# Kernel optimization log

Measured on AMD Instinct MI355X. Metric: run time of the kernel, lower is better.

Reference implementation:

```python
import jax, jax.numpy as jnp
import numpy as np
import math

NUM_HEADS = 8
FDIM = 64
NUM_BUCKETS = 32
MAX_DISTANCE = 128


def _relative_position_bucket(rel_pos, num_buckets=NUM_BUCKETS, max_distance=MAX_DISTANCE):
    nb = num_buckets // 2
    ret = (rel_pos >= 0).astype(jnp.int32) * nb
    n = jnp.abs(rel_pos)
    max_exact = nb // 2
    is_small = n < max_exact
    # safe log: clamp n to >=1 where large-branch is unused
    val_large = max_exact + (
        jnp.log(jnp.maximum(n, 1).astype(jnp.float32) / max_exact)
        / math.log(max_distance / max_exact) * (nb - max_exact)
    ).astype(jnp.int32)
    val_large = jnp.minimum(val_large, nb - 1)
    return ret + jnp.where(is_small, n, val_large)


def setup_inputs() -> dict:
    key = jax.random.key(0)
    k = jax.random.split(key, 5)
    B, Nin, F, T = 4, 64, FDIM, 1024
    N = NUM_HEADS * FDIM
    x = jax.random.normal(k[0], (B, Nin, F, T), dtype=jnp.float32)
    # kaiming_normal: std = 1/sqrt(fan_in)
    w_in = jax.random.normal(k[1], (NUM_HEADS, Nin), dtype=jnp.float32) / np.sqrt(Nin)
    w_qk = jax.random.normal(k[2], (2 * N, N), dtype=jnp.float32) / np.sqrt(N)
    w_out = jax.random.normal(k[3], (Nin, NUM_HEADS), dtype=jnp.float32) / np.sqrt(NUM_HEADS)
    rel_bias = jax.random.normal(k[4], (NUM_BUCKETS, NUM_HEADS), dtype=jnp.float32) * 0.02
    return {"x": x, "w_in": w_in, "w_qk": w_qk, "w_out": w_out, "rel_bias": rel_bias}


def reference(x, w_in, w_qk, w_out, rel_bias):
    B, Nin, F, T = x.shape
    h, f = NUM_HEADS, FDIM
    scale = f ** (-0.5)
    # proj_in: 1x1 conv2d Nin -> h
    xi = jnp.einsum('bcft,hc->bhft', x, w_in)          # [B,h,F,T]
    xr = xi.reshape(B, h * f, T)                        # b (h f) t
    v = xr.reshape(B, h, f, T).transpose(0, 1, 3, 2)    # [B,h,T,f]
    # qk: 1x1 conv1d N -> 2N
    qk = jnp.einsum('bct,dc->bdt', xr, w_qk)            # [B,2N,T]
    qk = qk.reshape(B, h, 2 * f, T).transpose(0, 1, 3, 2)  # [B,h,T,2f]
    q, k = qk[..., :f], qk[..., f:]
    sim = jnp.einsum('bhnd,bhmd->bhnm', q, k)           # [B,h,T,T]
    # relative position bias
    q_pos = jnp.arange(T)
    k_pos = jnp.arange(T)
    rel = k_pos[None, :] - q_pos[:, None]               # [T,T]
    buckets = _relative_position_bucket(rel)
    bias = rel_bias[buckets]                            # [T,T,h]
    bias = bias.transpose(2, 0, 1)[None]                # [1,h,T,T]
    sim = (sim + bias) * scale
    attn = jax.nn.softmax(sim, axis=-1)
    out = jnp.einsum('bhnm,bhmd->bhnd', attn, v)        # [B,h,T,f]
    out = out.transpose(0, 1, 3, 2)                     # [B,h,f,T]
    out = jnp.einsum('bhft,ch->bcft', out, w_out)       # [B,Nin,F,T]
    return out
```

## Files before the change

### kernel.cpp

```cpp
#include <hip/hip_runtime.h>
#include <math.h>

#define QSCALE 0.18033688011112042f

typedef __attribute__((ext_vector_type(4))) float  f32x4;
typedef __attribute__((ext_vector_type(2))) float  f32x2;
typedef __attribute__((ext_vector_type(8))) short  bf16x8;
typedef __attribute__((ext_vector_type(4))) short  bf16x4;
typedef __attribute__((ext_vector_type(4))) int    i32x4;

static __device__ __forceinline__ short f2bf(float f) {
    union { float f; unsigned u; } v; v.f = f;
    unsigned r = v.u + 0x7fffu + ((v.u >> 16) & 1u);
    return (short)(r >> 16);
}
static __device__ __forceinline__ int pk2bf(float a, float b) {
    return ((int)f2bf(a) & 0xffff) | ((int)f2bf(b) << 16);
}

#define MFMA16(A,B,C) __builtin_amdgcn_mfma_f32_16x16x32_bf16(A, B, C, 0, 0, 0)

__global__ void k_prep(const float* __restrict__ wqk, short* __restrict__ wqk_b) {
    int i = blockIdx.x * 256 + threadIdx.x;
    int D = i >> 9;
    float s = (D & 64) ? 1.0f : QSCALE;
    wqk_b[i] = f2bf(wqk[i] * s);
}

__global__ __launch_bounds__(256) void k_proj_in(
    const float* __restrict__ x, const float* __restrict__ w_in,
    short* __restrict__ xi_v, short* __restrict__ xr_t)
{
    __shared__ float w_s[512];
    __shared__ __align__(16) short tr[64 * 72];
    int tid = threadIdx.x;
    int tx = tid & 31, fy = tid >> 5;
    int tb = blockIdx.x, fb = blockIdx.y, b = blockIdx.z;
    w_s[tid] = w_in[tid & 511];
    w_s[(tid + 256) & 511] = w_in[(tid + 256) & 511];
    __syncthreads();

    int f = fb * 8 + fy;
    int t = tb * 64 + tx * 2;
    float acc[8][2];
    #pragma unroll
    for (int h = 0; h < 8; h++) { acc[h][0] = 0.f; acc[h][1] = 0.f; }

    const float* xp = x + ((size_t)b * 64 * 64 + (size_t)f) * 1024 + t;
    f32x2 buf[8];
    #pragma unroll
    for (int i = 0; i < 8; i++) buf[i] = *(const f32x2*)&xp[(size_t)i * 65536];
    #pragma unroll
    for (int c8 = 0; c8 < 64; c8 += 8) {
        f32x2 cur[8];
        #pragma unroll
        for (int i = 0; i < 8; i++) cur[i] = buf[i];
        if (c8 + 8 < 64) {
            #pragma unroll
            for (int i = 0; i < 8; i++)
                buf[i] = *(const f32x2*)&xp[(size_t)(c8 + 8 + i) * 65536];
        }
        #pragma unroll
        for (int i = 0; i < 8; i++)
            #pragma unroll
            for (int h = 0; h < 8; h++) {
                float wv = w_s[h * 64 + c8 + i];
                acc[h][0] = fmaf(cur[i][0], wv, acc[h][0]);
                acc[h][1] = fmaf(cur[i][1], wv, acc[h][1]);
            }
    }
    #pragma unroll
    for (int h = 0; h < 8; h++)
        *(int*)&xi_v[(((size_t)b * 8 + h) * 64 + f) * 1024 + t] = pk2bf(acc[h][0], acc[h][1]);
    #pragma unroll
    for (int h = 0; h < 8; h++) {
        tr[(tx * 2 + 0) * 72 + h * 8 + fy] = f2bf(acc[h][0]);
        tr[(tx * 2 + 1) * 72 + h * 8 + fy] = f2bf(acc[h][1]);
    }
    __syncthreads();
    int h2 = tid & 7, trow = tid >> 3;
    #pragma unroll
    for (int i = 0; i < 2; i++) {
        int t2 = trow + i * 32;
        i32x4 v = *(const i32x4*)&tr[t2 * 72 + h2 * 8];
        *(i32x4*)&xr_t[((size_t)b * 1024 + tb * 64 + t2) * 512 + h2 * 64 + fb * 8] = v;
    }
}

__global__ __launch_bounds__(256, 4) void k_qk(
    const short* __restrict__ wqk_b, const short* __restrict__ xr_t,
    short* __restrict__ qk_t)
{
    __shared__ __align__(16) short As[64 * 72];
    __shared__ __align__(16) short Bs[64 * 72];
    int tid = threadIdx.x;
    int w = tid >> 6, lane = tid & 63;
    int quad = lane >> 4, l16 = lane & 15;
    int t0 = blockIdx.x * 64;
    int Dt = blockIdx.y;
    int b  = blockIdx.z;

    f32x4 acc[4];
    #pragma unroll
    for (int tt = 0; tt < 4; tt++) acc[tt] = (f32x4){0.f,0.f,0.f,0.f};

    const short* Ag = wqk_b + (size_t)Dt * 64 * 512;
    const short* Bg = xr_t + ((size_t)b * 1024 + t0) * 512;

    int s_row = tid >> 2, s_col = (tid & 3) * 16;

    for (int kk = 0; kk < 512; kk += 64) {
        __syncthreads();
        #pragma unroll
        for (int i = 0; i < 2; i++) {
            *(i32x4*)&As[s_row * 72 + s_col + i * 8] =
                *(const i32x4*)&Ag[(size_t)s_row * 512 + kk + s_col + i * 8];
            *(i32x4*)&Bs[s_row * 72 + s_col + i * 8] =
                *(const i32x4*)&Bg[(size_t)s_row * 512 + kk + s_col + i * 8];
        }
        __syncthreads();
        bf16x8 af[2];
        #pragma unroll
        for (int kc = 0; kc < 2; kc++)
            af[kc] = *(const bf16x8*)&As[(w * 16 + l16) * 72 + kc * 32 + quad * 8];
        #pragma unroll
        for (int tt = 0; tt < 4; tt++) {
            bf16x8 bf0 = *(const bf16x8*)&Bs[(tt * 16 + l16) * 72 + quad * 8];
            bf16x8 bf1 = *(const bf16x8*)&Bs[(tt * 16 + l16) * 72 + 32 + quad * 8];
            acc[tt] = MFMA16(af[0], bf0, acc[tt]);
            acc[tt] = MFMA16(af[1], bf1, acc[tt]);
        }
    }
    int h = Dt >> 1;
    int d2 = (Dt & 1) * 64 + w * 16 + quad * 4;
    #pragma unroll
    for (int tt = 0; tt < 4; tt++) {
        bf16x4 pk;
        pk.x = f2bf(acc[tt][0]); pk.y = f2bf(acc[tt][1]);
        pk.z = f2bf(acc[tt][2]); pk.w = f2bf(acc[tt][3]);
        int t = t0 + tt * 16 + l16;
        *(bf16x4*)&qk_t[(((size_t)b * 8 + h) * 1024 + t) * 128 + d2] = pk;
    }
}

__global__ __launch_bounds__(256, 4) void k_attn(
    const short* __restrict__ qk_t, const short* __restrict__ xi_v,
    const float* __restrict__ rel_bias, float* __restrict__ o_part,
    float* __restrict__ lsum)
{
    __shared__ __align__(16) short Ks[64 * 72];
    __shared__ __align__(16) short Vs[64 * 72];
    __shared__ __align__(16) short Ps[4][16 * 72];
    __shared__ float elut[2048];
    int tid = threadIdx.x;
    int w = tid >> 6, lane = tid & 63;
    int quad = lane >> 4, l16 = lane & 15;
    int nb = blockIdx.x, bh = blockIdx.y, mh = blockIdx.z;
    int h = bh & 7;
    int n_base = nb * 64;

    for (int i = tid; i < 2047; i += 256) {
        int rel = i - 1023;
        int ret = (rel >= 0) ? 16 : 0;
        int na = rel < 0 ? -rel : rel;
        int idx;
        if (na < 8) idx = ret + na;
        else {
            int vl = 8 + (int)(log2f((float)na * 0.125f) * 2.0f);
            vl = vl > 15 ? 15 : vl;
            idx = ret + vl;
        }
        elut[i] = exp2f(rel_bias[idx * 8 + h] * QSCALE);
    }

    const short* qb = qk_t + (size_t)bh * (1024 * 128);
    const short* vb = xi_v + (size_t)bh * (64 * 1024);

    bf16x8 qf[2];
    #pragma unroll
    for (int kk = 0; kk < 2; kk++)
        qf[kk] = *(const bf16x8*)&qb[(size_t)(n_base + w * 16 + l16) * 128 + kk * 32 + quad * 8];

    f32x4 acc_o[4];
    #pragma unroll
    for (int dt = 0; dt < 4; dt++) acc_o[dt] = (f32x4){0.f,0.f,0.f,0.f};
    float l_st = 0.f;

    int srow = tid >> 2;
    int soff = (tid & 3) * 16;
    int m0 = mh * 512;
    i32x4 gk[2], gv[2];
    #pragma unroll
    for (int i = 0; i < 2; i++) {
        gk[i] = *(const i32x4*)&qb[(size_t)(m0 + srow) * 128 + 64 + soff + i * 8];
        gv[i] = *(const i32x4*)&vb[(size_t)srow * 1024 + m0 + soff + i * 8];
    }

    __syncthreads();

    #pragma unroll 1
    for (int it = 0; it < 8; it++) {
        *(i32x4*)&Ks[srow * 72 + soff]     = gk[0];
        *(i32x4*)&Ks[srow * 72 + soff + 8] = gk[1];
        *(i32x4*)&Vs[srow * 72 + soff]     = gv[0];
        *(i32x4*)&Vs[srow * 72 + soff + 8] = gv[1];
        __syncthreads();
        if (it < 7) {
            int m1 = m0 + 64;
            #pragma unroll
            for (int i = 0; i < 2; i++) {
                gk[i] = *(const i32x4*)&qb[(size_t)(m1 + srow) * 128 + 64 + soff + i * 8];
                gv[i] = *(const i32x4*)&vb[(size_t)srow * 1024 + m1 + soff + i * 8];
            }
        }

        f32x4 s[4];
        #pragma unroll
        for (int mt = 0; mt < 4; mt++) {
            bf16x8 kf0 = *(const bf16x8*)&Ks[(mt * 16 + l16) * 72 + quad * 8];
            bf16x8 kf1 = *(const bf16x8*)&Ks[(mt * 16 + l16) * 72 + 32 + quad * 8];
            f32x4 tacc = (f32x4){0.f,0.f,0.f,0.f};
            tacc = MFMA16(kf0, qf[0], tacc);
            tacc = MFMA16(kf1, qf[1], tacc);
            s[mt] = tacc;
        }

        int n = n_base + w * 16 + l16;
        #pragma unroll
        for (int mt = 0; mt < 4; mt++) {
            int rel0 = m0 + mt * 16 + quad * 4 - n + 1023;
            #pragma unroll
            for (int j = 0; j < 4; j++) {
                float p = exp2f(s[mt][j]) * elut[rel0 + j];
                s[mt][j] = p;
                l_st += p;
            }
        }
        #pragma unroll
        for (int mt = 0; mt < 4; mt++) {
            bf16x4 pk;
            pk.x = f2bf(s[mt][0]); pk.y = f2bf(s[mt][1]);
            pk.z = f2bf(s[mt][2]); pk.w = f2bf(s[mt][3]);
            *(bf16x4*)&Ps[w][l16 * 72 + mt * 16 + quad * 4] = pk;
        }
        #pragma unroll
        for (int si = 0; si < 2; si++) {
            bf16x8 pf = *(const bf16x8*)&Ps[w][l16 * 72 + si * 32 + quad * 8];
            #pragma unroll
            for (int dt = 0; dt < 4; dt++) {
                bf16x8 vf = *(const bf16x8*)&Vs[(dt * 16 + l16) * 72 + si * 32 + quad * 8];
                acc_o[dt] = MFMA16(pf, vf, acc_o[dt]);
            }
        }
        m0 += 64;
        __syncthreads();
    }
    #pragma unroll
    for (int dt = 0; dt < 4; dt++)
        *(f32x4*)&o_part[(((size_t)mh * 32 + bh) * 64 + dt * 16 + l16) * 1024 + n_base + w * 16 + quad * 4] = acc_o[dt];
    l_st += __shfl_xor(l_st, 16);
    l_st += __shfl_xor(l_st, 32);
    if (quad == 0)
        lsum[((size_t)bh * 2 + mh) * 1024 + n_base + w * 16 + l16] = l_st;
}

__global__ __launch_bounds__(512) void k_proj_out(
    const float* __restrict__ o_part, const float* __restrict__ lsum,
    const float* __restrict__ w_out, float* __restrict__ out)
{
    __shared__ float w_s[512];
    __shared__ float o_s[8][64];
    int tid = threadIdx.x;
    int tx = tid & 63, ty = tid >> 6;
    int tb = blockIdx.x, f = blockIdx.y, b = blockIdx.z;
    w_s[tid] = w_out[tid];
    int t = tb * 64 + tx;
    int bh = b * 8 + ty;
    float l0 = lsum[((size_t)bh * 2 + 0) * 1024 + t];
    float l1 = lsum[((size_t)bh * 2 + 1) * 1024 + t];
    float o0 = o_part[((size_t)(0 * 32 + bh) * 64 + f) * 1024 + t];
    float o1 = o_part[((size_t)(1 * 32 + bh) * 64 + f) * 1024 + t];
    o_s[ty][tx] = (o0 + o1) / (l0 + l1);
    __syncthreads();
    float ov[8];
    #pragma unroll
    for (int hh = 0; hh < 8; hh++) ov[hh] = o_s[hh][tx];
    #pragma unroll
    for (int j = 0; j < 8; j++) {
        int c = ty * 8 + j;
        float a = 0.f;
        #pragma unroll
        for (int hh = 0; hh < 8; hh++) a = fmaf(ov[hh], w_s[c * 8 + hh], a);
        out[(((size_t)b * 64 + c) * 64 + f) * 1024 + t] = a;
    }
}

extern "C" void kernel_launch(void* const* d_in, const int* in_sizes, int n_in,
                              void* d_out, int out_size, void* d_ws, size_t ws_size,
                              hipStream_t stream)
{
    const float* x        = (const float*)d_in[0];
    const float* w_in     = (const float*)d_in[1];
    const float* w_qk     = (const float*)d_in[2];
    const float* w_out    = (const float*)d_in[3];
    const float* rel_bias = (const float*)d_in[4];
    float* out = (float*)d_out;

    char* ws = (char*)d_ws;
    short* wqk_b  = (short*)(ws);
    short* xi_v   = (short*)(ws + (size_t)1  * (1 << 20));
    short* xr_t   = (short*)(ws + (size_t)5  * (1 << 20));
    short* qk_t   = (short*)(ws + (size_t)9  * (1 << 20));
    float* o_part = (float*)(ws + (size_t)17 * (1 << 20));
    float* lsum   = (float*)(ws + (size_t)33 * (1 << 20));

    hipLaunchKernelGGL(k_prep,     dim3(2048),       dim3(256), 0, stream, w_qk, wqk_b);
    hipLaunchKernelGGL(k_proj_in,  dim3(16, 8, 4),   dim3(256), 0, stream, x, w_in, xi_v, xr_t);
    hipLaunchKernelGGL(k_qk,       dim3(16, 16, 4),  dim3(256), 0, stream, wqk_b, xr_t, qk_t);
    hipLaunchKernelGGL(k_attn,     dim3(16, 32, 2),  dim3(256), 0, stream, qk_t, xi_v, rel_bias, o_part, lsum);
    hipLaunchKernelGGL(k_proj_out, dim3(16, 64, 4),  dim3(512), 0, stream, o_part, lsum, w_out, out);
}
```

Baseline: 162.2 us.

## Fuse weight bf16 conversion into QK GEMM and drop attention key-split

Removes the separate weight-prep kernel by converting fp32 w_qk to scaled bf16 inside the QK GEMM's shared-memory load. The attention kernel no longer splits keys into two halves. Each block now loops over all 1024 keys and normalizes its output by the row sum itself. A remapped 1D grid with an XCD-aware block swizzle replaces the 3D grid. This cuts one launch, the partial-output write/read and the combine step in proj_out. In exchange the attention grid halves to 512 blocks and each block's serial loop gets longer.

```diff
diff --git a/kernel.cpp b/kernel.cpp
--- a/kernel.cpp
+++ b/kernel.cpp
@@ -19,13 +19,6 @@
 }
 
 #define MFMA16(A,B,C) __builtin_amdgcn_mfma_f32_16x16x32_bf16(A, B, C, 0, 0, 0)
-
-__global__ void k_prep(const float* __restrict__ wqk, short* __restrict__ wqk_b) {
-    int i = blockIdx.x * 256 + threadIdx.x;
-    int D = i >> 9;
-    float s = (D & 64) ? 1.0f : QSCALE;
-    wqk_b[i] = f2bf(wqk[i] * s);
-}
 
 __global__ __launch_bounds__(256) void k_proj_in(
     const float* __restrict__ x, const float* __restrict__ w_in,
@@ -88,7 +81,7 @@
 }
 
 __global__ __launch_bounds__(256, 4) void k_qk(
-    const short* __restrict__ wqk_b, const short* __restrict__ xr_t,
+    const float* __restrict__ wqk, const short* __restrict__ xr_t,
     short* __restrict__ qk_t)
 {
     __shared__ __align__(16) short As[64 * 72];
@@ -104,20 +97,28 @@
     #pragma unroll
     for (int tt = 0; tt < 4; tt++) acc[tt] = (f32x4){0.f,0.f,0.f,0.f};
 
-    const short* Ag = wqk_b + (size_t)Dt * 64 * 512;
+    int s_row = tid >> 2, s_col = (tid & 3) * 16;
+    const float* Ag = wqk + ((size_t)Dt * 64 + s_row) * 512;
     const short* Bg = xr_t + ((size_t)b * 1024 + t0) * 512;
-
-    int s_row = tid >> 2, s_col = (tid & 3) * 16;
+    float s = (Dt & 1) ? 1.0f : QSCALE;
 
     for (int kk = 0; kk < 512; kk += 64) {
         __syncthreads();
-        #pragma unroll
-        for (int i = 0; i < 2; i++) {
-            *(i32x4*)&As[s_row * 72 + s_col + i * 8] =
-                *(const i32x4*)&Ag[(size_t)s_row * 512 + kk + s_col + i * 8];
-            *(i32x4*)&Bs[s_row * 72 + s_col + i * 8] =
-                *(const i32x4*)&Bg[(size_t)s_row * 512 + kk + s_col + i * 8];
-        }
+        f32x4 a0 = *(const f32x4*)&Ag[kk + s_col];
+        f32x4 a1 = *(const f32x4*)&Ag[kk + s_col + 4];
+        f32x4 a2 = *(const f32x4*)&Ag[kk + s_col + 8];
+        f32x4 a3 = *(const f32x4*)&Ag[kk + s_col + 12];
+        i32x4 w0, w1;
+        w0[0] = pk2bf(a0[0]*s, a0[1]*s); w0[1] = pk2bf(a0[2]*s, a0[3]*s);
+        w0[2] = pk2bf(a1[0]*s, a1[1]*s); w0[3] = pk2bf(a1[2]*s, a1[3]*s);
+        w1[0] = pk2bf(a2[0]*s, a2[1]*s); w1[1] = pk2bf(a2[2]*s, a2[3]*s);
+        w1[2] = pk2bf(a3[0]*s, a3[1]*s); w1[3] = pk2bf(a3[2]*s, a3[3]*s);
+        *(i32x4*)&As[s_row * 72 + s_col]     = w0;
+        *(i32x4*)&As[s_row * 72 + s_col + 8] = w1;
+        *(i32x4*)&Bs[s_row * 72 + s_col] =
+            *(const i32x4*)&Bg[(size_t)s_row * 512 + kk + s_col];
+        *(i32x4*)&Bs[s_row * 72 + s_col + 8] =
+            *(const i32x4*)&Bg[(size_t)s_row * 512 + kk + s_col + 8];
         __syncthreads();
         bf16x8 af[2];
         #pragma unroll
@@ -145,8 +146,7 @@
 
 __global__ __launch_bounds__(256, 4) void k_attn(
     const short* __restrict__ qk_t, const short* __restrict__ xi_v,
-    const float* __restrict__ rel_bias, float* __restrict__ o_part,
-    float* __restrict__ lsum)
+    const float* __restrict__ rel_bias, float* __restrict__ o_n)
 {
     __shared__ __align__(16) short Ks[64 * 72];
     __shared__ __align__(16) short Vs[64 * 72];
@@ -155,7 +155,9 @@
     int tid = threadIdx.x;
     int w = tid >> 6, lane = tid & 63;
     int quad = lane >> 4, l16 = lane & 15;
-    int nb = blockIdx.x, bh = blockIdx.y, mh = blockIdx.z;
+    int bid = blockIdx.x;
+    int wg = (bid & 7) * 64 + (bid >> 3);
+    int nb = wg & 15, bh = wg >> 4;
     int h = bh & 7;
     int n_base = nb * 64;
 
@@ -188,7 +190,7 @@
 
     int srow = tid >> 2;
     int soff = (tid & 3) * 16;
-    int m0 = mh * 512;
+    int m0 = 0;
     i32x4 gk[2], gv[2];
     #pragma unroll
     for (int i = 0; i < 2; i++) {
@@ -199,13 +201,13 @@
     __syncthreads();
 
     #pragma unroll 1
-    for (int it = 0; it < 8; it++) {
+    for (int it = 0; it < 16; it++) {
         *(i32x4*)&Ks[srow * 72 + soff]     = gk[0];
         *(i32x4*)&Ks[srow * 72 + soff + 8] = gk[1];
         *(i32x4*)&Vs[srow * 72 + soff]     = gv[0];
         *(i32x4*)&Vs[srow * 72 + soff + 8] = gv[1];
         __syncthreads();
-        if (it < 7) {
+        if (it < 15) {
             int m1 = m0 + 64;
             #pragma unroll
             for (int i = 0; i < 2; i++) {
@@ -255,18 +257,24 @@
         m0 += 64;
         __syncthreads();
     }
-    #pragma unroll
-    for (int dt = 0; dt < 4; dt++)
-        *(f32x4*)&o_part[(((size_t)mh * 32 + bh) * 64 + dt * 16 + l16) * 1024 + n_base + w * 16 + quad * 4] = acc_o[dt];
     l_st += __shfl_xor(l_st, 16);
     l_st += __shfl_xor(l_st, 32);
-    if (quad == 0)
-        lsum[((size_t)bh * 2 + mh) * 1024 + n_base + w * 16 + l16] = l_st;
+    float linv[4];
+    #pragma unroll
+    for (int j = 0; j < 4; j++)
+        linv[j] = 1.0f / __shfl(l_st, quad * 4 + j);
+    #pragma unroll
+    for (int dt = 0; dt < 4; dt++) {
+        f32x4 ov;
+        #pragma unroll
+        for (int j = 0; j < 4; j++) ov[j] = acc_o[dt][j] * linv[j];
+        *(f32x4*)&o_n[(((size_t)bh) * 64 + dt * 16 + l16) * 1024 + n_base + w * 16 + quad * 4] = ov;
+    }
 }
 
 __global__ __launch_bounds__(512) void k_proj_out(
-    const float* __restrict__ o_part, const float* __restrict__ lsum,
-    const float* __restrict__ w_out, float* __restrict__ out)
+    const float* __restrict__ o_n, const float* __restrict__ w_out,
+    float* __restrict__ out)
 {
     __shared__ float w_s[512];
     __shared__ float o_s[8][64];
@@ -275,12 +283,7 @@
     int tb = blockIdx.x, f = blockIdx.y, b = blockIdx.z;
     w_s[tid] = w_out[tid];
     int t = tb * 64 + tx;
-    int bh = b * 8 + ty;
-    float l0 = lsum[((size_t)bh * 2 + 0) * 1024 + t];
-    float l1 = lsum[((size_t)bh * 2 + 1) * 1024 + t];
-    float o0 = o_part[((size_t)(0 * 32 + bh) * 64 + f) * 1024 + t];
-    float o1 = o_part[((size_t)(1 * 32 + bh) * 64 + f) * 1024 + t];
-    o_s[ty][tx] = (o0 + o1) / (l0 + l1);
+    o_s[ty][tx] = o_n[((size_t)(b * 8 + ty) * 64 + f) * 1024 + t];
     __syncthreads();
     float ov[8];
     #pragma unroll
@@ -307,16 +310,13 @@
     float* out = (float*)d_out;
 
     char* ws = (char*)d_ws;
-    short* wqk_b  = (short*)(ws);
-    short* xi_v   = (short*)(ws + (size_t)1  * (1 << 20));
-    short* xr_t   = (short*)(ws + (size_t)5  * (1 << 20));
-    short* qk_t   = (short*)(ws + (size_t)9  * (1 << 20));
-    float* o_part = (float*)(ws + (size_t)17 * (1 << 20));
-    float* lsum   = (float*)(ws + (size_t)33 * (1 << 20));
-
-    hipLaunchKernelGGL(k_prep,     dim3(2048),       dim3(256), 0, stream, w_qk, wqk_b);
+    short* xi_v = (short*)(ws);
+    short* xr_t = (short*)(ws + (size_t)4  * (1 << 20));
+    short* qk_t = (short*)(ws + (size_t)8  * (1 << 20));
+    float* o_n  = (float*)(ws + (size_t)16 * (1 << 20));
+
     hipLaunchKernelGGL(k_proj_in,  dim3(16, 8, 4),   dim3(256), 0, stream, x, w_in, xi_v, xr_t);
-    hipLaunchKernelGGL(k_qk,       dim3(16, 16, 4),  dim3(256), 0, stream, wqk_b, xr_t, qk_t);
-    hipLaunchKernelGGL(k_attn,     dim3(16, 32, 2),  dim3(256), 0, stream, qk_t, xi_v, rel_bias, o_part, lsum);
-    hipLaunchKernelGGL(k_proj_out, dim3(16, 64, 4),  dim3(512), 0, stream, o_part, lsum, w_out, out);
-}
+    hipLaunchKernelGGL(k_qk,       dim3(16, 16, 4),  dim3(256), 0, stream, w_qk, xr_t, qk_t);
+    hipLaunchKernelGGL(k_attn,     dim3(512),        dim3(256), 0, stream, qk_t, xi_v, rel_bias, o_n);
+    hipLaunchKernelGGL(k_proj_out, dim3(16, 64, 4),  dim3(512), 0, stream, o_n, w_out, out);
+}
```

Result: slower. 165.9 us (+2.2%).
